# Optimization experiments

Hardware: AMD Instinct MI355X
Metric: run time of the kernel (lower is better)

## Reference

```python
import jax, jax.numpy as jnp
import numpy as np

B, C, P, NG, NCLS, HID, N, IMG = 2, 256, 7, 2, 81, 1024, 512, 800
STRIDES = [4, 8, 16, 32]
SCALE = 56.0  # roi_map_level_scale


def _roi_align(feat, rois, pooled, scale, ng):
    """torchvision-legacy (aligned=False) ROI Align. feat [B,C,H,W], rois [N,5]."""
    Bf, Cf, H, W = feat.shape
    ft = jnp.transpose(feat, (0, 2, 3, 1))  # [B,H,W,C]
    b = rois[:, 0].astype(jnp.int32)
    x1, y1, x2, y2 = (rois[:, i] * scale for i in (1, 2, 3, 4))
    rw = jnp.maximum(x2 - x1, 1.0)
    rh = jnp.maximum(y2 - y1, 1.0)
    # sample grid per output bin: ng points per axis, centered in sub-bins
    g = (jnp.arange(pooled)[:, None] + (jnp.arange(ng)[None, :] + 0.5) / ng).reshape(-1)  # [P*ng]
    ys = y1[:, None] + g[None, :] * (rh / pooled)[:, None]  # [N,S]
    xs = x1[:, None] + g[None, :] * (rw / pooled)[:, None]

    def axis(coord, size):
        valid = (coord >= -1.0) & (coord <= size)
        c = jnp.clip(coord, 0.0, size - 1)
        lo = jnp.floor(c).astype(jnp.int32)
        hi = jnp.minimum(lo + 1, size - 1)
        return valid, lo, hi, c - lo

    vy, ylo, yhi, fy = axis(ys, H)
    vx, xlo, xhi, fx = axis(xs, W)
    bb = b[:, None, None]

    def gather(yi, xi):
        return ft[bb, yi[:, :, None], xi[:, None, :], :]  # [N,S,S,C]

    wy = fy[:, :, None, None]
    wx = fx[:, None, :, None]
    val = ((1 - wy) * (1 - wx) * gather(ylo, xlo) + (1 - wy) * wx * gather(ylo, xhi)
           + wy * (1 - wx) * gather(yhi, xlo) + wy * wx * gather(yhi, xhi))
    val = jnp.where((vy[:, :, None] & vx[:, None, :])[..., None], val, 0.0)
    val = val.reshape(-1, pooled, ng, pooled, ng, Cf).mean(axis=(2, 4))  # [N,P,P,C]
    return jnp.transpose(val, (0, 3, 1, 2))  # [N,C,P,P]


def setup_inputs() -> dict:
    key = jax.random.key(0)
    ks = jax.random.split(key, 16)
    feats = {}
    for i, s in enumerate(STRIDES):
        hw = IMG // s
        feats[f"p{i+2}"] = jax.random.normal(ks[i], (B, C, hw, hw), jnp.float32)
    # realistic proposals: batch idx + boxes with sizes 16..512 px
    bidx = jax.random.randint(ks[4], (N,), 0, B).astype(jnp.float32)
    sw = 2.0 ** jax.random.uniform(ks[5], (N,), minval=4.0, maxval=9.0)
    sh = 2.0 ** jax.random.uniform(ks[6], (N,), minval=4.0, maxval=9.0)
    x1 = jax.random.uniform(ks[7], (N,)) * (IMG - sw)
    y1 = jax.random.uniform(ks[8], (N,)) * (IMG - sh)
    rois = jnp.stack([bidx, x1, y1, x1 + sw - 1, y1 + sh - 1], axis=1)
    D = C * P * P
    inp = dict(feats, rois=rois,
               w1=0.01 * jax.random.normal(ks[9], (HID, D), jnp.float32),
               b1=jnp.zeros((HID,), jnp.float32),
               w2=0.01 * jax.random.normal(ks[10], (HID, HID), jnp.float32),
               b2=jnp.zeros((HID,), jnp.float32),
               w_cls=0.01 * jax.random.normal(ks[11], (NCLS, HID), jnp.float32),
               b_cls=jnp.zeros((NCLS,), jnp.float32),
               w_reg=0.001 * jax.random.normal(ks[12], (NCLS * 4, HID), jnp.float32),
               b_reg=jnp.zeros((NCLS * 4,), jnp.float32))
    return inp


def reference(p2, p3, p4, p5, rois, w1, b1, w2, b2, w_cls, b_cls, w_reg, b_reg):
    feats = [p2, p3, p4, p5]
    # FPN level assignment (same math as torch: log2(sqrt(hw)/scale + 1e-6), floor, clamp)
    rh = rois[:, 4] - rois[:, 2] + 1
    rw = rois[:, 3] - rois[:, 1] + 1
    levels = jnp.clip(jnp.floor(jnp.log2(jnp.sqrt(rh * rw) / SCALE + 1e-6)), 0, 3).astype(jnp.int32)
    # dispatch: compute each ROI on its assigned level (masked combine == gather/sort-scatter)
    pooled = jnp.zeros((rois.shape[0], C, P, P), rois.dtype)
    for l, feat in enumerate(feats):
        pl = _roi_align(feat, rois, P, 1.0 / STRIDES[l], NG)
        pooled = pooled + jnp.where((levels == l)[:, None, None, None], pl, 0.0)
    x = pooled.reshape(pooled.shape[0], -1)  # [N, C*P*P]
    x = jax.nn.relu(x @ w1.T + b1)
    x = jax.nn.relu(x @ w2.T + b2)
    x_cls = x @ w_cls.T + b_cls
    x_reg = x @ w_reg.T + b_reg  # TEST mode, not class-agnostic: no gather
    cls_probs = jax.nn.softmax(x_cls, axis=1)
    rois_out = rois.reshape(B, -1, 5)
    cls_probs = cls_probs.reshape(B, rois_out.shape[1], -1)
    bbox_preds = x_reg.reshape(B, rois_out.shape[1], -1)
    return rois_out, cls_probs, bbox_preds
```

## Files before the change

### kernel.cpp

```cpp
#include <hip/hip_runtime.h>
#include <hip/hip_bf16.h>
#include <math.h>

#define NROI   512
#define CCH    256
#define POOLP  7
#define DDIM   12544
#define HIDN   1024
#define NCLS   81
#define NREG   324
#define NHEAD  512
#define OUT_ROIS   2560
#define OUT_CLS    (512*81)

typedef __attribute__((ext_vector_type(4))) float f32x4;
typedef __attribute__((ext_vector_type(8))) short bf16x8;

static __device__ __forceinline__ unsigned short f2bf(float x) {
    __hip_bfloat16 h = __float2bfloat16(x);
    return *reinterpret_cast<unsigned short*>(&h);
}
static __device__ __forceinline__ float bf2f(unsigned short u) {
    unsigned int b = ((unsigned int)u) << 16;
    return *reinterpret_cast<float*>(&b);
}

#define PS_B0 10
#define PS_B1 (PS_B0 + 768)
#define PS_B2 (PS_B1 + 1024)
#define PS_B3 (PS_B2 + 1024)
__global__ __launch_bounds__(256) void prep_small_k(const float* __restrict__ rois,
                                                    const float* __restrict__ w2,
                                                    const float* __restrict__ wc,
                                                    const float* __restrict__ wr,
                                                    float* __restrict__ out,
                                                    float* __restrict__ accz,
                                                    unsigned short* __restrict__ w2b,
                                                    unsigned short* __restrict__ whd) {
    int bid = blockIdx.x, t = threadIdx.x;
    if (bid < PS_B0) {
        int i = bid * 256 + t;
        if (i < OUT_ROIS) out[i] = rois[i];
    } else if (bid < PS_B1) {
        int i = (bid - PS_B0) * 256 + t;
        ((float4*)accz)[i] = make_float4(0.f, 0.f, 0.f, 0.f);
    } else if (bid < PS_B2) {
        int i = (bid - PS_B1) * 256 + t;
        float4 v = ((const float4*)w2)[i];
        ushort4 o;
        o.x = f2bf(v.x); o.y = f2bf(v.y); o.z = f2bf(v.z); o.w = f2bf(v.w);
        ((ushort4*)w2b)[i] = o;
    } else {
        int i2 = (bid - PS_B2) * 256 + t;
        int r = i2 >> 9, c = (i2 & 511) << 1;
        float v0, v1;
        if (r < NCLS)             { v0 = wc[r * HIDN + c]; v1 = wc[r * HIDN + c + 1]; }
        else if (r < NCLS + NREG) { v0 = wr[(r - NCLS) * HIDN + c]; v1 = wr[(r - NCLS) * HIDN + c + 1]; }
        else                      { v0 = 0.f; v1 = 0.f; }
        ((unsigned int*)whd)[i2] = (unsigned int)f2bf(v0) | ((unsigned int)f2bf(v1) << 16);
    }
}

__global__ __launch_bounds__(256) void permute_w1_k(const float* __restrict__ w1,
                                                    unsigned short* __restrict__ w1b) {
    __shared__ unsigned short lw[49 * 258];
    int n = blockIdx.x, t = threadIdx.x;
    const float* src = w1 + (size_t)n * DDIM;
    for (int k = t; k < DDIM; k += 256) {
        int c = k / 49;
        int s = k - c * 49;
        lw[s * 258 + c] = f2bf(src[k]);
    }
    __syncthreads();
    unsigned int* dst = (unsigned int*)(w1b + (size_t)n * DDIM);
    for (int j2 = t; j2 < DDIM / 2; j2 += 256) {
        int s = j2 >> 7, c2 = (j2 & 127) << 1;
        dst[j2] = lw[s * 258 + c2] | ((unsigned int)lw[s * 258 + c2 + 1] << 16);
    }
}

__global__ __launch_bounds__(256) void transpose_k(const float* __restrict__ p2,
                                                   const float* __restrict__ p3,
                                                   const float* __restrict__ p4,
                                                   const float* __restrict__ p5,
                                                   unsigned short* __restrict__ f0,
                                                   unsigned short* __restrict__ f1,
                                                   unsigned short* __restrict__ f2,
                                                   unsigned short* __restrict__ f3) {
    __shared__ float sm[64][65];
    int xb = blockIdx.x;
    const float* in; unsigned short* op; int S, base;
    if (xb < 625)      { in = p2; op = f0; S = 40000; base = 0; }
    else if (xb < 782) { in = p3; op = f1; S = 10000; base = 625; }
    else if (xb < 822) { in = p4; op = f2; S = 2500;  base = 782; }
    else               { in = p5; op = f3; S = 625;   base = 822; }
    int s0 = (xb - base) * 64;
    int c0 = blockIdx.y * 64;
    int b  = blockIdx.z;
    int t  = threadIdx.x;

    int sL = (t & 15) * 4, cc0 = t >> 4;
    bool vec = (s0 + 64 <= S) && ((S & 3) == 0);
#pragma unroll
    for (int i = 0; i < 4; i++) {
        int cc = cc0 + i * 16;
        const float* src = in + ((size_t)(b * CCH + c0 + cc)) * S + s0 + sL;
        if (vec) {
            float4 v = *(const float4*)src;
            sm[sL + 0][cc] = v.x; sm[sL + 1][cc] = v.y;
            sm[sL + 2][cc] = v.z; sm[sL + 3][cc] = v.w;
        } else {
#pragma unroll
            for (int j = 0; j < 4; j++)
                sm[sL + j][cc] = (s0 + sL + j < S) ? src[j] : 0.f;
        }
    }
    __syncthreads();

    int cq = (t & 15) * 4, sr = t >> 4;
#pragma unroll
    for (int i = 0; i < 4; i++) {
        int s = sr + i * 16;
        if (s0 + s < S) {
            float a = sm[s][cq], bb = sm[s][cq + 1], c = sm[s][cq + 2], d = sm[s][cq + 3];
            uint2 v;
            v.x = (unsigned int)f2bf(a) | ((unsigned int)f2bf(bb) << 16);
            v.y = (unsigned int)f2bf(c) | ((unsigned int)f2bf(d) << 16);
            *(uint2*)(op + ((size_t)b * S + s0 + s) * CCH + c0 + cq) = v;
        }
    }
}

__global__ __launch_bounds__(256) void roi_align_k(const unsigned short* __restrict__ f0,
                                                   const unsigned short* __restrict__ f1,
                                                   const unsigned short* __restrict__ f2,
                                                   const unsigned short* __restrict__ f3,
                                                   const float* __restrict__ rois,
                                                   unsigned short* __restrict__ xpool) {
    __shared__ float s_f[16];
    __shared__ int   s_lo[16], s_hi[16], s_v[16];

    int py = blockIdx.x, r = blockIdx.y, t = threadIdx.x;

    float r0  = rois[r * 5 + 0];
    float rx1 = rois[r * 5 + 1], ry1 = rois[r * 5 + 2];
    float rx2 = rois[r * 5 + 3], ry2 = rois[r * 5 + 4];
    int b = (int)r0;

    float aw = rx2 - rx1 + 1.f, ah = ry2 - ry1 + 1.f;
    float lvf = floorf(log2f(sqrtf(ah * aw) / 56.f + 1e-6f));
    int lv = (int)fminf(fmaxf(lvf, 0.f), 3.f);

    const unsigned short* F = (lv == 0) ? f0 : (lv == 1) ? f1 : (lv == 2) ? f2 : f3;
    int HW      = (lv == 0) ? 200 : (lv == 1) ? 100 : (lv == 2) ? 50 : 25;
    float scale = (lv == 0) ? 0.25f : (lv == 1) ? 0.125f : (lv == 2) ? 0.0625f : 0.03125f;

    float x1 = rx1 * scale, yy1 = ry1 * scale;
    float x2 = rx2 * scale, yy2 = ry2 * scale;
    float rw = fmaxf(x2 - x1, 1.f), rh = fmaxf(yy2 - yy1, 1.f);

    if (t < 16) {
        bool isY = t < 2;
        float coord;
        if (isY) {
            float g = (float)py + ((float)t + 0.5f) * 0.5f;
            coord = yy1 + g * (rh * (1.f / 7.f));
        } else {
            int j = t - 2;
            float g = (float)(j >> 1) + ((float)(j & 1) + 0.5f) * 0.5f;
            coord = x1 + g * (rw * (1.f / 7.f));
        }
        int vld = (coord >= -1.f && coord <= (float)HW) ? 1 : 0;
        float c = fminf(fmaxf(coord, 0.f), (float)(HW - 1));
        int lo  = (int)floorf(c);
        int hi  = min(lo + 1, HW - 1);
        s_v[t] = vld; s_lo[t] = lo; s_hi[t] = hi; s_f[t] = c - (float)lo;
    }
    __syncthreads();

    const unsigned short* Fb = F + ((size_t)b * HW * HW) * CCH + t;
    size_t obase = (size_t)r * DDIM + py * 7 * 256 + t;

    for (int px = 0; px < POOLP; px++) {
        float acc = 0.f;
#pragma unroll
        for (int s = 0; s < 4; s++) {
            int iy = s >> 1;
            int ix = px * 2 + (s & 1);
            int vy = s_v[iy], vx = s_v[2 + ix];
            if (vy & vx) {
                float fy = s_f[iy], fx = s_f[2 + ix];
                int ylo = s_lo[iy], yhi = s_hi[iy];
                int xlo = s_lo[2 + ix], xhi = s_hi[2 + ix];
                float v00 = bf2f(Fb[((size_t)ylo * HW + xlo) * CCH]);
                float v01 = bf2f(Fb[((size_t)ylo * HW + xhi) * CCH]);
                float v10 = bf2f(Fb[((size_t)yhi * HW + xlo) * CCH]);
                float v11 = bf2f(Fb[((size_t)yhi * HW + xhi) * CCH]);
                acc += (1.f - fy) * ((1.f - fx) * v00 + fx * v01)
                     + fy * ((1.f - fx) * v10 + fx * v11);
            }
        }
        xpool[obase + px * 256] = f2bf(acc * 0.25f);
    }
}

__global__ __launch_bounds__(256) void roi_align_nchw_k(const float* __restrict__ f0,
                                                        const float* __restrict__ f1,
                                                        const float* __restrict__ f2,
                                                        const float* __restrict__ f3,
                                                        const float* __restrict__ rois,
                                                        unsigned short* __restrict__ xpool) {
    __shared__ float s_f[16];
    __shared__ int   s_lo[16], s_hi[16], s_v[16];
    int py = blockIdx.x, r = blockIdx.y, t = threadIdx.x;
    float r0  = rois[r * 5 + 0];
    float rx1 = rois[r * 5 + 1], ry1 = rois[r * 5 + 2];
    float rx2 = rois[r * 5 + 3], ry2 = rois[r * 5 + 4];
    int b = (int)r0;
    float aw = rx2 - rx1 + 1.f, ah = ry2 - ry1 + 1.f;
    float lvf = floorf(log2f(sqrtf(ah * aw) / 56.f + 1e-6f));
    int lv = (int)fminf(fmaxf(lvf, 0.f), 3.f);
    const float* F = (lv == 0) ? f0 : (lv == 1) ? f1 : (lv == 2) ? f2 : f3;
    int HW      = (lv == 0) ? 200 : (lv == 1) ? 100 : (lv == 2) ? 50 : 25;
    float scale = (lv == 0) ? 0.25f : (lv == 1) ? 0.125f : (lv == 2) ? 0.0625f : 0.03125f;
    float x1 = rx1 * scale, yy1 = ry1 * scale;
    float x2 = rx2 * scale, yy2 = ry2 * scale;
    float rw = fmaxf(x2 - x1, 1.f), rh = fmaxf(yy2 - yy1, 1.f);
    if (t < 16) {
        bool isY = t < 2;
        float coord;
        if (isY) {
            float g = (float)py + ((float)t + 0.5f) * 0.5f;
            coord = yy1 + g * (rh * (1.f / 7.f));
        } else {
            int j = t - 2;
            float g = (float)(j >> 1) + ((float)(j & 1) + 0.5f) * 0.5f;
            coord = x1 + g * (rw * (1.f / 7.f));
        }
        int vld = (coord >= -1.f && coord <= (float)HW) ? 1 : 0;
        float c = fminf(fmaxf(coord, 0.f), (float)(HW - 1));
        int lo  = (int)floorf(c);
        int hi  = min(lo + 1, HW - 1);
        s_v[t] = vld; s_lo[t] = lo; s_hi[t] = hi; s_f[t] = c - (float)lo;
    }
    __syncthreads();
    const float* Fb = F + ((size_t)b * CCH + t) * HW * HW;
    size_t obase = (size_t)r * DDIM + py * 7 * 256 + t;
    for (int px = 0; px < POOLP; px++) {
        float acc = 0.f;
#pragma unroll
        for (int s = 0; s < 4; s++) {
            int iy = s >> 1, ix = px * 2 + (s & 1);
            int vy = s_v[iy], vx = s_v[2 + ix];
            if (vy & vx) {
                float fy = s_f[iy], fx = s_f[2 + ix];
                int ylo = s_lo[iy], yhi = s_hi[iy];
                int xlo = s_lo[2 + ix], xhi = s_hi[2 + ix];
                float v00 = Fb[(size_t)ylo * HW + xlo];
                float v01 = Fb[(size_t)ylo * HW + xhi];
                float v10 = Fb[(size_t)yhi * HW + xlo];
                float v11 = Fb[(size_t)yhi * HW + xhi];
                acc += (1.f - fy) * ((1.f - fx) * v00 + fx * v01)
                     + fy * ((1.f - fx) * v10 + fx * v11);
            }
        }
        xpool[obase + px * 256] = f2bf(acc * 0.25f);
    }
}

__global__ __launch_bounds__(256) void gemm_bf16_k(const unsigned short* __restrict__ A,
                                                   const unsigned short* __restrict__ W,
                                                   float* __restrict__ Cacc,
                                                   int M, int N, int K, int kchunk) {
    __shared__ __align__(16) unsigned short As[2][8][64][8];
    __shared__ __align__(16) unsigned short Ws[2][8][64][8];

    int t = threadIdx.x;
    int lane = t & 63, wid = t >> 6;
    int m0 = blockIdx.y * 64, n0 = blockIdx.x * 64;
    int k0 = blockIdx.z * kchunk;
    int wm = (wid >> 1) * 32, wn = (wid & 1) * 32;
    int fr = lane & 15, kg = lane >> 4;
    int nsteps = kchunk >> 6;

    f32x4 acc[2][2] = {};

    const unsigned short* Arow = A + (size_t)(m0 + lane) * K;
    const unsigned short* Wrow = W + (size_t)(n0 + lane) * K;

    auto stage = [&](int buf, int kb) {
#pragma unroll
        for (int i = 0; i < 2; i++) {
            int c = wid * 2 + i;
            __builtin_amdgcn_global_load_lds(
                (const __attribute__((address_space(1))) void*)(Arow + kb + c * 8),
                (__attribute__((address_space(3))) void*)(&As[buf][c][0][0]), 16, 0, 0);
            __builtin_amdgcn_global_load_lds(
                (const __attribute__((address_space(1))) void*)(Wrow + kb + c * 8),
                (__attribute__((address_space(3))) void*)(&Ws[buf][c][0][0]), 16, 0, 0);
        }
    };

    stage(0, k0);
    __syncthreads();
    int cur = 0;
    for (int tt = 0; tt < nsteps; ++tt) {
        if (tt + 1 < nsteps) stage(cur ^ 1, k0 + (tt + 1) * 64);
#pragma unroll
        for (int h = 0; h < 2; h++) {
            bf16x8 a0 = *(const bf16x8*)(&As[cur][h * 4 + kg][wm + fr][0]);
            bf16x8 a1 = *(const bf16x8*)(&As[cur][h * 4 + kg][wm + 16 + fr][0]);
            bf16x8 b0 = *(const bf16x8*)(&Ws[cur][h * 4 + kg][wn + fr][0]);
            bf16x8 b1 = *(const bf16x8*)(&Ws[cur][h * 4 + kg][wn + 16 + fr][0]);
            acc[0][0] = __builtin_amdgcn_mfma_f32_16x16x32_bf16(a0, b0, acc[0][0], 0, 0, 0);
            acc[0][1] = __builtin_amdgcn_mfma_f32_16x16x32_bf16(a0, b1, acc[0][1], 0, 0, 0);
            acc[1][0] = __builtin_amdgcn_mfma_f32_16x16x32_bf16(a1, b0, acc[1][0], 0, 0, 0);
            acc[1][1] = __builtin_amdgcn_mfma_f32_16x16x32_bf16(a1, b1, acc[1][1], 0, 0, 0);
        }
        __syncthreads();
        cur ^= 1;
    }

    int row = m0 + wm + (lane >> 4) * 4;
    int col = n0 + wn + fr;
#pragma unroll
    for (int fm = 0; fm < 2; fm++)
#pragma unroll
        for (int fn = 0; fn < 2; fn++)
#pragma unroll
            for (int r = 0; r < 4; r++)
                atomicAdd(&Cacc[(size_t)(row + fm * 16 + r) * N + col + fn * 16],
                          acc[fm][fn][r]);
}

__global__ __launch_bounds__(256) void gemm128_bf16_k(const unsigned short* __restrict__ A,
                                                      const unsigned short* __restrict__ W,
                                                      float* __restrict__ Cp,
                                                      int M, int N, int K, int kchunk) {
    __shared__ __align__(16) unsigned short As[2][8][128][8];
    __shared__ __align__(16) unsigned short Ws[2][8][128][8];

    int lin  = blockIdx.x;
    int nb   = (lin & 7) * 56 + (lin >> 3);
    int tile = nb / 14, bz = nb - tile * 14;
    int bx = tile & 7, by = tile >> 3;

    int t = threadIdx.x;
    int lane = t & 63, wid = t >> 6;
    int m0 = by * 128, n0 = bx * 128;
    int k0 = bz * kchunk;
    int wm = (wid >> 1) * 64, wn = (wid & 1) * 64;
    int fr = lane & 15, kg = lane >> 4;
    int nsteps = kchunk >> 6;

    f32x4 acc[4][4] = {};

    auto stage = [&](int buf, int kb) {
#pragma unroll
        for (int i = 0; i < 4; i++) {
            int c   = wid * 4 + i;
            int kgc = c >> 1;
            int r0w = (c & 1) * 64;
            __builtin_amdgcn_global_load_lds(
                (const __attribute__((address_space(1))) void*)
                    (A + (size_t)(m0 + r0w + lane) * K + kb + kgc * 8),
                (__attribute__((address_space(3))) void*)(&As[buf][kgc][r0w][0]), 16, 0, 0);
            __builtin_amdgcn_global_load_lds(
                (const __attribute__((address_space(1))) void*)
                    (W + (size_t)(n0 + r0w + lane) * K + kb + kgc * 8),
                (__attribute__((address_space(3))) void*)(&Ws[buf][kgc][r0w][0]), 16, 0, 0);
        }
    };

    stage(0, k0);
    __syncthreads();
    int cur = 0;
    for (int tt = 0; tt < nsteps; ++tt) {
        if (tt + 1 < nsteps) stage(cur ^ 1, k0 + (tt + 1) * 64);
#pragma unroll
        for (int h = 0; h < 2; h++) {
            bf16x8 av[4], bv[4];
#pragma unroll
            for (int f = 0; f < 4; f++) {
                av[f] = *(const bf16x8*)(&As[cur][h * 4 + kg][wm + f * 16 + fr][0]);
                bv[f] = *(const bf16x8*)(&Ws[cur][h * 4 + kg][wn + f * 16 + fr][0]);
            }
#pragma unroll
            for (int fm = 0; fm < 4; fm++)
#pragma unroll
                for (int fn = 0; fn < 4; fn++)
                    acc[fm][fn] = __builtin_amdgcn_mfma_f32_16x16x32_bf16(
                        av[fm], bv[fn], acc[fm][fn], 0, 0, 0);
        }
        __syncthreads();
        cur ^= 1;
    }

    float* Cout = Cp + (size_t)bz * ((size_t)M * N);
    int row = m0 + wm + (lane >> 4) * 4;
    int col = n0 + wn + fr;
#pragma unroll
    for (int fm = 0; fm < 4; fm++)
#pragma unroll
        for (int fn = 0; fn < 4; fn++)
#pragma unroll
            for (int r = 0; r < 4; r++)
                Cout[(size_t)(row + fm * 16 + r) * N + col + fn * 16] = acc[fm][fn][r];
}

__global__ __launch_bounds__(256) void fc_ep_k(const float* __restrict__ Cp,
                                               const float* __restrict__ bias,
                                               unsigned short* __restrict__ dst,
                                               int MN, int ks) {
    int i = blockIdx.x * 256 + threadIdx.x;
    if (i >= MN) return;
    float s = 0.f;
    for (int p = 0; p < ks; p++) s += Cp[(size_t)p * MN + i];
    s = fmaxf(s + bias[i & (HIDN - 1)], 0.f);
    dst[i] = f2bf(s);
}

__global__ void head_ep_k(const float* __restrict__ hf,
                          const float* __restrict__ bc,
                          const float* __restrict__ br,
                          float* __restrict__ out) {
    int r = blockIdx.x, l = threadIdx.x;
    const float* row = hf + (size_t)r * NHEAD;

    float* reg = out + OUT_ROIS + OUT_CLS + (size_t)r * NREG;
    for (int j = l; j < NREG; j += 64) reg[j] = row[NCLS + j] + br[j];

    float v0 = row[l] + bc[l];
    float v1 = (l + 64 < NCLS) ? row[l + 64] + bc[l + 64] : -INFINITY;
    float m = fmaxf(v0, v1);
#pragma unroll
    for (int o = 32; o; o >>= 1) m = fmaxf(m, __shfl_xor(m, o));
    float e0 = __expf(v0 - m);
    float e1 = (l + 64 < NCLS) ? __expf(v1 - m) : 0.f;
    float s = e0 + e1;
#pragma unroll
    for (int o = 32; o; o >>= 1) s += __shfl_xor(s, o);
    float inv = 1.f / s;
    float* cls = out + OUT_ROIS + (size_t)r * NCLS;
    cls[l] = e0 * inv;
    if (l + 64 < NCLS) cls[l + 64] = e1 * inv;
}

extern "C" void kernel_launch(void* const* d_in, const int* in_sizes, int n_in,
                              void* d_out, int out_size, void* d_ws, size_t ws_size,
                              hipStream_t stream) {
    const float* p2   = (const float*)d_in[0];
    const float* p3   = (const float*)d_in[1];
    const float* p4   = (const float*)d_in[2];
    const float* p5   = (const float*)d_in[3];
    const float* rois = (const float*)d_in[4];
    const float* w1   = (const float*)d_in[5];
    const float* b1   = (const float*)d_in[6];
    const float* w2   = (const float*)d_in[7];
    const float* b2   = (const float*)d_in[8];
    const float* wc   = (const float*)d_in[9];
    const float* bc   = (const float*)d_in[10];
    const float* wr   = (const float*)d_in[11];
    const float* br   = (const float*)d_in[12];

    float* out = (float*)d_out;

    const int KS1 = 14;

    char* p = (char*)d_ws;
    auto alloc = [&](size_t bytes) { char* r = p; p += (bytes + 255) & ~(size_t)255; return r; };
    unsigned short* xpool = (unsigned short*)alloc((size_t)NROI * DDIM * 2);
    unsigned short* y1b   = (unsigned short*)alloc((size_t)NROI * HIDN * 2);
    unsigned short* y2b   = (unsigned short*)alloc((size_t)NROI * HIDN * 2);
    unsigned short* w1b   = (unsigned short*)alloc((size_t)HIDN * DDIM * 2);
    unsigned short* w2b   = (unsigned short*)alloc((size_t)HIDN * HIDN * 2);
    unsigned short* whd   = (unsigned short*)alloc((size_t)NHEAD * HIDN * 2);
    float*          accz  = (float*)alloc((size_t)(NROI * HIDN + NROI * NHEAD) * 4);
    unsigned short* ft0 = (unsigned short*)alloc((size_t)2 * 40000 * CCH * 2);
    unsigned short* ft1 = (unsigned short*)alloc((size_t)2 * 10000 * CCH * 2);
    unsigned short* ft2 = (unsigned short*)alloc((size_t)2 * 2500 * CCH * 2);
    unsigned short* ft3 = (unsigned short*)alloc((size_t)2 * 625 * CCH * 2);
    bool nhwc = (size_t)(p - (char*)d_ws) <= ws_size;

    float* y2f = accz;
    float* hf  = accz + (size_t)NROI * HIDN;
    float* part = (float*)ft0;

    prep_small_k<<<PS_B3, 256, 0, stream>>>(rois, w2, wc, wr, out, accz, w2b, whd);
    permute_w1_k<<<HIDN, 256, 0, stream>>>(w1, w1b);

    if (nhwc) {
        transpose_k<<<dim3(832, 4, 2), 256, 0, stream>>>(p2, p3, p4, p5,
                                                         ft0, ft1, ft2, ft3);
        roi_align_k<<<dim3(POOLP, NROI), 256, 0, stream>>>(ft0, ft1, ft2, ft3, rois, xpool);
    } else {
        roi_align_nchw_k<<<dim3(POOLP, NROI), 256, 0, stream>>>(p2, p3, p4, p5, rois, xpool);
    }

    gemm128_bf16_k<<<8 * 4 * KS1, 256, 0, stream>>>(
        xpool, w1b, part, NROI, HIDN, DDIM, DDIM / KS1);
    fc_ep_k<<<(NROI * HIDN + 255) / 256, 256, 0, stream>>>(part, b1, y1b, NROI * HIDN, KS1);

    gemm_bf16_k<<<dim3(HIDN / 64, NROI / 64, 2), 256, 0, stream>>>(
        y1b, w2b, y2f, NROI, HIDN, HIDN, HIDN / 2);
    fc_ep_k<<<(NROI * HIDN + 255) / 256, 256, 0, stream>>>(y2f, b2, y2b, NROI * HIDN, 1);

    gemm_bf16_k<<<dim3(NHEAD / 64, NROI / 64, 4), 256, 0, stream>>>(
        y2b, whd, hf, NROI, NHEAD, HIDN, HIDN / 4);
    head_ep_k<<<NROI, 64, 0, stream>>>(hf, bc, br, out);
}
```

Before: 156.8 us.

## Use atomic split-K for FC1, drop double buffering, widen transpose tiles

Result: slower. 204.6 us (+30.4%).

```diff
diff --git a/kernel.cpp b/kernel.cpp
--- a/kernel.cpp
+++ b/kernel.cpp
@@ -26,7 +26,7 @@
 }
 
 #define PS_B0 10
-#define PS_B1 (PS_B0 + 768)
+#define PS_B1 (PS_B0 + 1280)
 #define PS_B2 (PS_B1 + 1024)
 #define PS_B3 (PS_B2 + 1024)
 __global__ __launch_bounds__(256) void prep_small_k(const float* __restrict__ rois,
@@ -87,46 +87,48 @@
                                                    unsigned short* __restrict__ f1,
                                                    unsigned short* __restrict__ f2,
                                                    unsigned short* __restrict__ f3) {
-    __shared__ float sm[64][65];
-    int xb = blockIdx.x;
-    const float* in; unsigned short* op; int S, base;
-    if (xb < 625)      { in = p2; op = f0; S = 40000; base = 0; }
-    else if (xb < 782) { in = p3; op = f1; S = 10000; base = 625; }
-    else if (xb < 822) { in = p4; op = f2; S = 2500;  base = 782; }
-    else               { in = p5; op = f3; S = 625;   base = 822; }
-    int s0 = (xb - base) * 64;
-    int c0 = blockIdx.y * 64;
-    int b  = blockIdx.z;
+    __shared__ float sm[64][261];
+    int idx = blockIdx.x;
+    const float* in; unsigned short* op; int S, nS, base;
+    if (idx < 1250)      { in = p2; op = f0; S = 40000; nS = 625; base = 0; }
+    else if (idx < 1564) { in = p3; op = f1; S = 10000; nS = 157; base = 1250; }
+    else if (idx < 1644) { in = p4; op = f2; S = 2500;  nS = 40;  base = 1564; }
+    else                 { in = p5; op = f3; S = 625;   nS = 10;  base = 1644; }
+    int j  = idx - base;
+    int b  = j / nS;
+    int s0 = (j - b * nS) * 64;
     int t  = threadIdx.x;
 
-    int sL = (t & 15) * 4, cc0 = t >> 4;
-    bool vec = (s0 + 64 <= S) && ((S & 3) == 0);
-#pragma unroll
-    for (int i = 0; i < 4; i++) {
-        int cc = cc0 + i * 16;
-        const float* src = in + ((size_t)(b * CCH + c0 + cc)) * S + s0 + sL;
+    int k = t & 15, g = t >> 4;
+    bool vec = (s0 + 64 <= S);
+    const float* src0 = in + ((size_t)(b * CCH + g * 16)) * S + s0 + k * 4;
+#pragma unroll
+    for (int jj = 0; jj < 16; jj++) {
+        const float* src = src0 + (size_t)jj * S;
+        int c = g * 16 + jj;
         if (vec) {
             float4 v = *(const float4*)src;
-            sm[sL + 0][cc] = v.x; sm[sL + 1][cc] = v.y;
-            sm[sL + 2][cc] = v.z; sm[sL + 3][cc] = v.w;
+            sm[k * 4 + 0][c] = v.x; sm[k * 4 + 1][c] = v.y;
+            sm[k * 4 + 2][c] = v.z; sm[k * 4 + 3][c] = v.w;
         } else {
 #pragma unroll
-            for (int j = 0; j < 4; j++)
-                sm[sL + j][cc] = (s0 + sL + j < S) ? src[j] : 0.f;
+            for (int e = 0; e < 4; e++)
+                sm[k * 4 + e][c] = (s0 + k * 4 + e < S) ? src[e] : 0.f;
         }
     }
     __syncthreads();
 
-    int cq = (t & 15) * 4, sr = t >> 4;
-#pragma unroll
-    for (int i = 0; i < 4; i++) {
-        int s = sr + i * 16;
+    int L = t & 63, w = t >> 6;
+#pragma unroll
+    for (int i = 0; i < 16; i++) {
+        int s = w * 16 + i;
         if (s0 + s < S) {
-            float a = sm[s][cq], bb = sm[s][cq + 1], c = sm[s][cq + 2], d = sm[s][cq + 3];
+            float a = sm[s][4 * L], bb = sm[s][4 * L + 1];
+            float c = sm[s][4 * L + 2], d = sm[s][4 * L + 3];
             uint2 v;
             v.x = (unsigned int)f2bf(a) | ((unsigned int)f2bf(bb) << 16);
             v.y = (unsigned int)f2bf(c) | ((unsigned int)f2bf(d) << 16);
-            *(uint2*)(op + ((size_t)b * S + s0 + s) * CCH + c0 + cq) = v;
+            *(uint2*)(op + ((size_t)b * S + s0 + s) * CCH + 4 * L) = v;
         }
     }
 }
@@ -335,14 +337,14 @@
 
 __global__ __launch_bounds__(256) void gemm128_bf16_k(const unsigned short* __restrict__ A,
                                                       const unsigned short* __restrict__ W,
-                                                      float* __restrict__ Cp,
+                                                      float* __restrict__ Cacc,
                                                       int M, int N, int K, int kchunk) {
-    __shared__ __align__(16) unsigned short As[2][8][128][8];
-    __shared__ __align__(16) unsigned short Ws[2][8][128][8];
+    __shared__ __align__(16) unsigned short As[8][128][8];
+    __shared__ __align__(16) unsigned short Ws[8][128][8];
 
     int lin  = blockIdx.x;
-    int nb   = (lin & 7) * 56 + (lin >> 3);
-    int tile = nb / 14, bz = nb - tile * 14;
+    int nb   = (lin & 7) * 112 + (lin >> 3);
+    int tile = nb / 28, bz = nb - tile * 28;
     int bx = tile & 7, by = tile >> 3;
 
     int t = threadIdx.x;
@@ -351,11 +353,10 @@
     int k0 = bz * kchunk;
     int wm = (wid >> 1) * 64, wn = (wid & 1) * 64;
     int fr = lane & 15, kg = lane >> 4;
-    int nsteps = kchunk >> 6;
 
     f32x4 acc[4][4] = {};
 
-    auto stage = [&](int buf, int kb) {
+    for (int kb = k0; kb < k0 + kchunk; kb += 64) {
 #pragma unroll
         for (int i = 0; i < 4; i++) {
             int c   = wid * 4 + i;
@@ -364,26 +365,20 @@
             __builtin_amdgcn_global_load_lds(
                 (const __attribute__((address_space(1))) void*)
                     (A + (size_t)(m0 + r0w + lane) * K + kb + kgc * 8),
-                (__attribute__((address_space(3))) void*)(&As[buf][kgc][r0w][0]), 16, 0, 0);
+                (__attribute__((address_space(3))) void*)(&As[kgc][r0w][0]), 16, 0, 0);
             __builtin_amdgcn_global_load_lds(
                 (const __attribute__((address_space(1))) void*)
                     (W + (size_t)(n0 + r0w + lane) * K + kb + kgc * 8),
-                (__attribute__((address_space(3))) void*)(&Ws[buf][kgc][r0w][0]), 16, 0, 0);
-        }
-    };
-
-    stage(0, k0);
-    __syncthreads();
-    int cur = 0;
-    for (int tt = 0; tt < nsteps; ++tt) {
-        if (tt + 1 < nsteps) stage(cur ^ 1, k0 + (tt + 1) * 64);
+                (__attribute__((address_space(3))) void*)(&Ws[kgc][r0w][0]), 16, 0, 0);
+        }
+        __syncthreads();
 #pragma unroll
         for (int h = 0; h < 2; h++) {
             bf16x8 av[4], bv[4];
 #pragma unroll
             for (int f = 0; f < 4; f++) {
-                av[f] = *(const bf16x8*)(&As[cur][h * 4 + kg][wm + f * 16 + fr][0]);
-                bv[f] = *(const bf16x8*)(&Ws[cur][h * 4 + kg][wn + f * 16 + fr][0]);
+                av[f] = *(const bf16x8*)(&As[h * 4 + kg][wm + f * 16 + fr][0]);
+                bv[f] = *(const bf16x8*)(&Ws[h * 4 + kg][wn + f * 16 + fr][0]);
             }
 #pragma unroll
             for (int fm = 0; fm < 4; fm++)
@@ -393,10 +388,8 @@
                         av[fm], bv[fn], acc[fm][fn], 0, 0, 0);
         }
         __syncthreads();
-        cur ^= 1;
-    }
-
-    float* Cout = Cp + (size_t)bz * ((size_t)M * N);
+    }
+
     int row = m0 + wm + (lane >> 4) * 4;
     int col = n0 + wn + fr;
 #pragma unroll
@@ -405,18 +398,16 @@
         for (int fn = 0; fn < 4; fn++)
 #pragma unroll
             for (int r = 0; r < 4; r++)
-                Cout[(size_t)(row + fm * 16 + r) * N + col + fn * 16] = acc[fm][fn][r];
-}
-
-__global__ __launch_bounds__(256) void fc_ep_k(const float* __restrict__ Cp,
+                atomicAdd(&Cacc[(size_t)(row + fm * 16 + r) * N + col + fn * 16],
+                          acc[fm][fn][r]);
+}
+
+__global__ __launch_bounds__(256) void fc_ep_k(const float* __restrict__ acc,
                                                const float* __restrict__ bias,
-                                               unsigned short* __restrict__ dst,
-                                               int MN, int ks) {
+                                               unsigned short* __restrict__ dst, int MN) {
     int i = blockIdx.x * 256 + threadIdx.x;
     if (i >= MN) return;
-    float s = 0.f;
-    for (int p = 0; p < ks; p++) s += Cp[(size_t)p * MN + i];
-    s = fmaxf(s + bias[i & (HIDN - 1)], 0.f);
+    float s = fmaxf(acc[i] + bias[i & (HIDN - 1)], 0.f);
     dst[i] = f2bf(s);
 }
 
@@ -465,7 +456,7 @@
 
     float* out = (float*)d_out;
 
-    const int KS1 = 14;
+    const int KS1 = 28;
 
     char* p = (char*)d_ws;
     auto alloc = [&](size_t bytes) { char* r = p; p += (bytes + 255) & ~(size_t)255; return r; };
@@ -475,35 +466,34 @@
     unsigned short* w1b   = (unsigned short*)alloc((size_t)HIDN * DDIM * 2);
     unsigned short* w2b   = (unsigned short*)alloc((size_t)HIDN * HIDN * 2);
     unsigned short* whd   = (unsigned short*)alloc((size_t)NHEAD * HIDN * 2);
-    float*          accz  = (float*)alloc((size_t)(NROI * HIDN + NROI * NHEAD) * 4);
+    float*          accz  = (float*)alloc((size_t)(NROI * HIDN * 2 + NROI * NHEAD) * 4);
     unsigned short* ft0 = (unsigned short*)alloc((size_t)2 * 40000 * CCH * 2);
     unsigned short* ft1 = (unsigned short*)alloc((size_t)2 * 10000 * CCH * 2);
     unsigned short* ft2 = (unsigned short*)alloc((size_t)2 * 2500 * CCH * 2);
     unsigned short* ft3 = (unsigned short*)alloc((size_t)2 * 625 * CCH * 2);
     bool nhwc = (size_t)(p - (char*)d_ws) <= ws_size;
 
-    float* y2f = accz;
-    float* hf  = accz + (size_t)NROI * HIDN;
-    float* part = (float*)ft0;
+    float* y1f = accz;
+    float* y2f = accz + (size_t)NROI * HIDN;
+    float* hf  = accz + (size_t)NROI * HIDN * 2;
 
     prep_small_k<<<PS_B3, 256, 0, stream>>>(rois, w2, wc, wr, out, accz, w2b, whd);
     permute_w1_k<<<HIDN, 256, 0, stream>>>(w1, w1b);
 
     if (nhwc) {
-        transpose_k<<<dim3(832, 4, 2), 256, 0, stream>>>(p2, p3, p4, p5,
-                                                         ft0, ft1, ft2, ft3);
+        transpose_k<<<1664, 256, 0, stream>>>(p2, p3, p4, p5, ft0, ft1, ft2, ft3);
         roi_align_k<<<dim3(POOLP, NROI), 256, 0, stream>>>(ft0, ft1, ft2, ft3, rois, xpool);
     } else {
         roi_align_nchw_k<<<dim3(POOLP, NROI), 256, 0, stream>>>(p2, p3, p4, p5, rois, xpool);
     }
 
     gemm128_bf16_k<<<8 * 4 * KS1, 256, 0, stream>>>(
-        xpool, w1b, part, NROI, HIDN, DDIM, DDIM / KS1);
-    fc_ep_k<<<(NROI * HIDN + 255) / 256, 256, 0, stream>>>(part, b1, y1b, NROI * HIDN, KS1);
+        xpool, w1b, y1f, NROI, HIDN, DDIM, DDIM / KS1);
+    fc_ep_k<<<(NROI * HIDN + 255) / 256, 256, 0, stream>>>(y1f, b1, y1b, NROI * HIDN);
 
     gemm_bf16_k<<<dim3(HIDN / 64, NROI / 64, 2), 256, 0, stream>>>(
         y1b, w2b, y2f, NROI, HIDN, HIDN, HIDN / 2);
-    fc_ep_k<<<(NROI * HIDN + 255) / 256, 256, 0, stream>>>(y2f, b2, y2b, NROI * HIDN, 1);
+    fc_ep_k<<<(NROI * HIDN + 255) / 256, 256, 0, stream>>>(y2f, b2, y2b, NROI * HIDN);
 
     gemm_bf16_k<<<dim3(NHEAD / 64, NROI / 64, 4), 256, 0, stream>>>(
         y2b, whd, hf, NROI, NHEAD, HIDN, HIDN / 4);
```
